# Optimization experiments

Measured on AMD Instinct MI355X. Metric: run time of the kernel, lower is better.

## Reference

```python
import jax, jax.numpy as jnp
import numpy as np

NUM_HEADS = 4
HEAD_DIM = 64
IN_CH = 192
KERNEL_SIZES = (3, 5, 7, 9)  # per-head neighborhood size
NEG_INF = -1e30


def setup_inputs() -> dict:
    key = jax.random.key(0)
    k1, k2, k3 = jax.random.split(key, 3)
    x = jax.random.normal(k1, (8, IN_CH, 96, 96), dtype=jnp.float32)
    # QKV conv: out_channels = head_dim * num_heads * 3 = 768, 3x3, pad 1
    w_qkv = jax.random.normal(k2, (HEAD_DIM * NUM_HEADS * 3, IN_CH, 3, 3), dtype=jnp.float32) * 0.02
    b_qkv = jax.random.normal(k3, (HEAD_DIM * NUM_HEADS * 3,), dtype=jnp.float32) * 0.02
    return {"x": x, "w_qkv": w_qkv, "b_qkv": b_qkv}


def _neighborhood_attention(q, k, v, ksize):
    # q, k, v: [N, H, W, D]; KxK zero-padded neighborhood attention with
    # out-of-bounds positions masked out.
    N, H, W, D = q.shape
    pad = ksize // 2
    kp = jnp.pad(k, ((0, 0), (pad, pad), (pad, pad), (0, 0)))
    vp = jnp.pad(v, ((0, 0), (pad, pad), (pad, pad), (0, 0)))
    scale = 1.0 / np.sqrt(D).astype(np.float32)
    rows = jnp.arange(H)
    cols = jnp.arange(W)
    scores, masks = [], []
    for di in range(ksize):
        for dj in range(ksize):
            k_sh = kp[:, di:di + H, dj:dj + W, :]           # shifted keys
            scores.append(jnp.einsum('nhwd,nhwd->nhw', q, k_sh))
            rv = (rows + di - pad >= 0) & (rows + di - pad < H)   # [H]
            cv = (cols + dj - pad >= 0) & (cols + dj - pad < W)   # [W]
            masks.append(rv[:, None] & cv[None, :])               # [H, W]
    scores = jnp.stack(scores, axis=-1) * scale                   # [N,H,W,K2]
    mask = jnp.stack(masks, axis=-1)[None]                        # [1,H,W,K2]
    scores = jnp.where(mask, scores, NEG_INF)
    attn = jax.nn.softmax(scores, axis=-1)                        # [N,H,W,K2]
    out = jnp.zeros_like(q)
    t = 0
    for di in range(ksize):
        for dj in range(ksize):
            out = out + attn[..., t, None] * vp[:, di:di + H, dj:dj + W, :]
            t += 1
    return out  # [N,H,W,D]


def reference(x, w_qkv, b_qkv):
    # Dense QKV projection (Conv2d, stride 1, padding 1 == SAME for k=3)
    qkv = jax.lax.conv_general_dilated(
        x, w_qkv, window_strides=(1, 1), padding='SAME',
        dimension_numbers=('NCHW', 'OIHW', 'NCHW'))
    qkv = qkv + b_qkv[None, :, None, None]
    # transform_to_nhw1c: NCHW -> NHWC, then split channels into
    # num_heads blocks of 3*head_dim, each split into q, k, v.
    N, C, H, W = qkv.shape
    qkv = jnp.transpose(qkv, (0, 2, 3, 1)).reshape(N, H, W, NUM_HEADS, 3, HEAD_DIM)
    outs = []
    for h, ks in enumerate(KERNEL_SIZES):
        q = qkv[..., h, 0, :]
        k = qkv[..., h, 1, :]
        v = qkv[..., h, 2, :]
        o = _neighborhood_attention(q, k, v, ks)       # [N,H,W,D]
        outs.append(jnp.transpose(o, (0, 3, 1, 2)))    # transform_from_nhw1c -> NCHW
    return jnp.stack(outs, axis=0)  # [num_heads, N, D, H, W]
```

## Files before the change

### kernel.cpp

```cpp
#include <hip/hip_runtime.h>
#include <hip/hip_bf16.h>

#define NH 96
#define NW 96
#define NB 8
#define CIN 192
#define COUT 768
#define PH 98

typedef __attribute__((ext_vector_type(8))) unsigned short ushort8;
typedef __attribute__((ext_vector_type(8))) short bf16x8;
typedef __attribute__((ext_vector_type(4))) float f32x4;

static __device__ __forceinline__ unsigned short f2bf(float f) {
    unsigned int u = __float_as_uint(f);
    return (unsigned short)((u + 0x7fffu + ((u >> 16) & 1u)) >> 16);
}

typedef const __attribute__((address_space(1))) unsigned int gu32;
typedef __attribute__((address_space(3))) unsigned int lu32;
static __device__ __forceinline__ void gload16(const void* g, void* l) {
    __builtin_amdgcn_global_load_lds((gu32*)g, (lu32*)l, 16, 0, 0);
}

__global__ __launch_bounds__(256) void pack_x_kernel(
    const float* __restrict__ x, unsigned short* __restrict__ xp)
{
    __shared__ float tile[32][97];
    int bid = blockIdx.x;
    int ct = bid % 6; int y = (bid / 6) % NH; int n = bid / (6 * NH);
    int tid = threadIdx.x;
    int c0 = ct * 32;
    for (int i = tid; i < 32 * 96; i += 256) {
        int c = i / 96, xx = i % 96;
        tile[c][xx] = x[(((size_t)n * CIN + c0 + c) * NH + y) * NW + xx];
    }
    __syncthreads();
    for (int i = tid; i < 96 * 4; i += 256) {
        int xx = i >> 2, ch = i & 3;
        ushort8 pk;
#pragma unroll
        for (int j = 0; j < 8; ++j) pk[j] = f2bf(tile[ch * 8 + j][xx]);
        *(ushort8*)(xp + ((size_t)(n * PH + y + 1) * PH + xx + 1) * CIN + c0 + ch * 8) = pk;
    }
}

__global__ __launch_bounds__(256) void pack_w_kernel(
    const float* __restrict__ w, unsigned short* __restrict__ bw)
{
    __shared__ float ls[1728];
    int co = blockIdx.x; int tid = threadIdx.x;
    for (int i = tid; i < 1728; i += 256) ls[i] = w[(size_t)co * 1728 + i];
    __syncthreads();
    for (int i = tid; i < 1728; i += 256) {
        int sh = i / 192, ci = i % 192;
        bw[(size_t)co * 1728 + i] = f2bf(ls[ci * 9 + sh]);
    }
}

#define BUFSZ 24576

#define STAGE(S, BUF)                                                          \
    {                                                                          \
        int shift_ = (S) / 6, kk_ = (S) - shift_ * 6;                          \
        int aO_ = ((shift_ / 3) * PH + (shift_ % 3)) * CIN + kk_ * 32;         \
        int bO_ = (S) * 32;                                                    \
        gload16(srcA[0] + aO_, dstA[0] + (BUF));                               \
        gload16(srcA[1] + aO_, dstA[1] + (BUF));                               \
        _Pragma("unroll")                                                      \
        for (int i_ = 0; i_ < 4; ++i_)                                         \
            gload16(srcB[i_] + bO_, dstB[i_] + (BUF));                         \
    }

#define COMPUTE(CUR)                                                           \
    {                                                                          \
        bf16x8 af[8], bf[4];                                                   \
        _Pragma("unroll")                                                      \
        for (int m_ = 0; m_ < 8; ++m_)                                         \
            af[m_] = *(const bf16x8*)(smem + (CUR) + aoff[m_]);                \
        _Pragma("unroll")                                                      \
        for (int n_ = 0; n_ < 4; ++n_)                                         \
            bf[n_] = *(const bf16x8*)(smem + (CUR) + boff[n_]);                \
        __builtin_amdgcn_s_setprio(1);                                         \
        _Pragma("unroll")                                                      \
        for (int m_ = 0; m_ < 8; ++m_)                                         \
            _Pragma("unroll")                                                  \
            for (int n_ = 0; n_ < 4; ++n_)                                     \
                acc[m_][n_] = __builtin_amdgcn_mfma_f32_16x16x32_bf16(         \
                    af[m_], bf[n_], acc[m_][n_], 0, 0, 0);                     \
        __builtin_amdgcn_s_setprio(0);                                         \
    }

__global__ __launch_bounds__(256, 2) void conv_gemm_kernel(
    const unsigned short* __restrict__ xp, const unsigned short* __restrict__ bw,
    const float* __restrict__ bias, unsigned short* __restrict__ qkq,
    unsigned short* __restrict__ vt)
{
    __shared__ __align__(16) char smem[3 * BUFSZ];
    int bid = (blockIdx.x & 7) * 216 + (blockIdx.x >> 3);
    int brow = (bid / 3) * 128, bcol = (bid % 3) * 256;
    int tid = threadIdx.x, lane = tid & 63, wn = tid >> 6;

    const unsigned short* srcA[2];
    const unsigned short* srcB[4];
    char* dstA[2];
    char* dstB[4];
#pragma unroll
    for (int i = 0; i < 2; ++i) {
        int s = i * 256 + tid;
        int row = s >> 2, c = s & 3;
        int p = brow + row;
        int n = p / 9216; int rem = p - n * 9216;
        int y = rem / 96; int xx = rem - y * 96;
        int csw = (c ^ ((row >> 1) & 3)) << 3;
        srcA[i] = xp + ((size_t)(n * PH + y) * PH + xx) * CIN + csw;
        dstA[i] = smem + (i * 256 + (tid & ~63)) * 16;
    }
#pragma unroll
    for (int i = 0; i < 4; ++i) {
        int s = i * 256 + tid;
        int row = s >> 2, c = s & 3;
        int csw = (c ^ ((row >> 1) & 3)) << 3;
        srcB[i] = bw + (size_t)(bcol + row) * 1728 + csw;
        dstB[i] = smem + 8192 + (i * 256 + (tid & ~63)) * 16;
    }

    int aoff[8], boff[4];
#pragma unroll
    for (int m = 0; m < 8; ++m) {
        int rowA = m * 16 + (lane & 15);
        aoff[m] = rowA * 64 + (((lane >> 4) ^ ((rowA >> 1) & 3)) << 4);
    }
#pragma unroll
    for (int n = 0; n < 4; ++n) {
        int colB = wn * 64 + n * 16 + (lane & 15);
        boff[n] = 8192 + colB * 64 + (((lane >> 4) ^ ((colB >> 1) & 3)) << 4);
    }

    STAGE(0, 0);
    STAGE(1, BUFSZ);

    f32x4 acc[8][4] = {};

    for (int t = 0; t < 52; ++t) {
        asm volatile("s_waitcnt vmcnt(6)" ::: "memory");
        __builtin_amdgcn_s_barrier();
        STAGE(t + 2, ((t + 2) % 3) * BUFSZ);
        __builtin_amdgcn_sched_barrier(0);
        COMPUTE((t % 3) * BUFSZ);
    }
    asm volatile("s_waitcnt vmcnt(6)" ::: "memory");
    __builtin_amdgcn_s_barrier();
    COMPUTE((52 % 3) * BUFSZ);
    asm volatile("s_waitcnt vmcnt(0)" ::: "memory");
    __builtin_amdgcn_s_barrier();
    COMPUTE((53 % 3) * BUFSZ);

    __syncthreads();
    unsigned short* sc = (unsigned short*)smem;
    float bn[4];
#pragma unroll
    for (int n = 0; n < 4; ++n)
        bn[n] = bias[bcol + wn * 64 + n * 16 + (lane & 15)];
#pragma unroll
    for (int m = 0; m < 8; ++m)
#pragma unroll
        for (int n = 0; n < 4; ++n) {
            int col = wn * 64 + n * 16 + (lane & 15);
            int cabs = bcol + col;
            float scale = ((cabs % 192) < 64) ? 0.125f : 1.0f;
#pragma unroll
            for (int j = 0; j < 4; ++j) {
                int row = m * 16 + (lane >> 4) * 4 + j;
                sc[row * 256 + (col ^ ((row & 7) << 3))] =
                    f2bf((acc[m][n][j] + bn[n]) * scale);
            }
        }
    __syncthreads();
#pragma unroll
    for (int i = 0; i < 16; ++i) {
        int idx = i * 256 + tid;
        int row = idx >> 5, ch = idx & 31;
        int c0 = bcol + ch * 8;
        int r192 = c0 % 192;
        if (r192 < 128) {
            ushort8 pk = *(const ushort8*)(sc + row * 256 + ((ch * 8) ^ ((row & 7) << 3)));
            *(ushort8*)(qkq + (size_t)(brow + row) * 512 + (c0 / 192) * 128 + r192) = pk;
        }
    }
    int nblk = brow / 9216;
    int prem = brow - nblk * 9216;
#pragma unroll
    for (int h = 0; h < 4; ++h) {
        int lc = h * 192 + 128 - bcol;
        if (lc < 0 || lc > 192) continue;
        unsigned short* vth = vt + (size_t)h * 4718592;
#pragma unroll
        for (int it = 0; it < 4; ++it) {
            int i = it * 256 + tid;
            int d = i & 63, pxb = i >> 6;
            ushort8 pk;
#pragma unroll
            for (int j = 0; j < 8; ++j) {
                int px = pxb * 8 + j;
                pk[j] = sc[px * 256 + ((lc + d) ^ ((px & 7) << 3))];
            }
            *(ushort8*)(vth + ((size_t)(nblk * 64 + d)) * 9216 + prem + pxb * 8) = pk;
        }
    }
}

template<int KS>
static __device__ __forceinline__ void na_body(
    const unsigned short* __restrict__ qkq, const unsigned short* __restrict__ vt,
    float* __restrict__ out, int head, int bid, char* nsm)
{
    constexpr int PAD = KS / 2;
    float (*sO)[97] = (float(*)[97])nsm;
    int y = bid % 96, n = bid / 96;
    int tid = threadIdx.x;
    int wv = tid >> 6, lane = tid & 63;
    int g = lane >> 4, pix = lane & 15;
    int x0 = wv * 16;
    int x = x0 + pix;
    int W = x0 - 8;

    size_t qbase = ((size_t)((n * 96 + y) * 96 + x)) * 512 + (size_t)head * 128;
    bf16x8 qf0 = *(const bf16x8*)(qkq + qbase + g * 8);
    bf16x8 qf1 = *(const bf16x8*)(qkq + qbase + 32 + g * 8);
    asm volatile("s_waitcnt vmcnt(0)" ::: "memory");

    const size_t hoff = (size_t)head * 128 + 64;
#define STAGEK(DI, BUF)                                                        \
    {                                                                          \
        int iy_ = min(max(y + (DI) - PAD, 0), 95);                             \
        size_t rb_ = ((size_t)((n * 96 + iy_) * 96)) * 512 + hoff;             \
        _Pragma("unroll")                                                      \
        for (int i_ = 0; i_ < 2; ++i_) {                                       \
            int ch_ = i_ * 384 + tid;                                          \
            int xx_ = ch_ >> 3, c8_ = (ch_ & 7) ^ (xx_ & 7);                   \
            gload16(qkq + rb_ + (size_t)xx_ * 512 + c8_ * 8,                   \
                    nsm + (BUF) * 12288 + (i_ * 384 + (tid & ~63)) * 16);      \
        }                                                                      \
    }

    STAGEK(0, 0);
    STAGEK(1, 1);

    f32x4 s[KS][2];
#pragma unroll
    for (int di = 0; di < KS; ++di)
#pragma unroll
        for (int kt = 0; kt < 2; ++kt)
#pragma unroll
            for (int r = 0; r < 4; ++r) s[di][kt][r] = -1e30f;

#pragma unroll
    for (int di = 0; di < KS; ++di) {
        if (di < KS - 1) asm volatile("s_waitcnt vmcnt(2)" ::: "memory");
        else             asm volatile("s_waitcnt vmcnt(0)" ::: "memory");
        __builtin_amdgcn_s_barrier();
        if (di + 2 < KS) STAGEK(di + 2, (di + 2) % 3);
        int iy = y + di - PAD;
        if (iy < 0 || iy >= 96) continue;
        const char* kb = nsm + (di % 3) * 12288;
#pragma unroll
        for (int kt = 0; kt < 2; ++kt) {
            int kix_l = W + kt * 16 + pix;
            int ixc = min(max(kix_l, 0), 95);
            const char* kr = kb + ixc * 128;
            bf16x8 kf0 = *(const bf16x8*)(kr + ((g ^ (ixc & 7)) << 4));
            bf16x8 kf1 = *(const bf16x8*)(kr + (((4 + g) ^ (ixc & 7)) << 4));
            f32x4 t = {};
            t = __builtin_amdgcn_mfma_f32_16x16x32_bf16(kf0, qf0, t, 0, 0, 0);
            t = __builtin_amdgcn_mfma_f32_16x16x32_bf16(kf1, qf1, t, 0, 0, 0);
#pragma unroll
            for (int r = 0; r < 4; ++r) {
                int kix = W + kt * 16 + g * 4 + r;
                bool valid = ((unsigned)(kix - x + PAD) <= (unsigned)(2 * PAD)) &&
                             ((unsigned)kix < 96u);
                s[di][kt][r] = valid ? t[r] : -1e30f;
            }
        }
    }

    float m = -3.0e38f;
#pragma unroll
    for (int di = 0; di < KS; ++di)
#pragma unroll
        for (int kt = 0; kt < 2; ++kt)
#pragma unroll
            for (int r = 0; r < 4; ++r) m = fmaxf(m, s[di][kt][r]);
    m = fmaxf(m, __shfl_xor(m, 16, 64));
    m = fmaxf(m, __shfl_xor(m, 32, 64));
    float l = 0.f;
#pragma unroll
    for (int di = 0; di < KS; ++di)
#pragma unroll
        for (int kt = 0; kt < 2; ++kt)
#pragma unroll
            for (int r = 0; r < 4; ++r) {
                float p = __expf(s[di][kt][r] - m);
                s[di][kt][r] = p;
                l += p;
            }
    l += __shfl_xor(l, 16, 64);
    l += __shfl_xor(l, 32, 64);

    f32x4 O[4] = {};
    int addrA = ((2 * (g & 1)) * 16 + pix) * 4;
    int addrB = addrA + 64;
    bool kthi = (g >> 1) != 0;
#pragma unroll
    for (int di = 0; di < KS; ++di) {
        int iy = y + di - PAD;
        if (iy < 0 || iy >= 96) continue;
        unsigned int w0[2], w1[2];
#pragma unroll
        for (int kt = 0; kt < 2; ++kt) {
            asm("v_cvt_pk_bf16_f32 %0, %1, %2"
                : "=v"(w0[kt]) : "v"(s[di][kt][0]), "v"(s[di][kt][1]));
            asm("v_cvt_pk_bf16_f32 %0, %1, %2"
                : "=v"(w1[kt]) : "v"(s[di][kt][2]), "v"(s[di][kt][3]));
        }
        int a0 = __builtin_amdgcn_ds_bpermute(addrA, (int)w0[0]);
        int b0 = __builtin_amdgcn_ds_bpermute(addrA, (int)w0[1]);
        int a1 = __builtin_amdgcn_ds_bpermute(addrA, (int)w1[0]);
        int b1 = __builtin_amdgcn_ds_bpermute(addrA, (int)w1[1]);
        int a2 = __builtin_amdgcn_ds_bpermute(addrB, (int)w0[0]);
        int b2 = __builtin_amdgcn_ds_bpermute(addrB, (int)w0[1]);
        int a3 = __builtin_amdgcn_ds_bpermute(addrB, (int)w1[0]);
        int b3 = __builtin_amdgcn_ds_bpermute(addrB, (int)w1[1]);
        union { int u[4]; bf16x8 v; } pa;
        pa.u[0] = kthi ? b0 : a0;
        pa.u[1] = kthi ? b1 : a1;
        pa.u[2] = kthi ? b2 : a2;
        pa.u[3] = kthi ? b3 : a3;
#pragma unroll
        for (int dc = 0; dc < 4; ++dc) {
            long voff = ((long)((n * 64 + dc * 16 + pix) * 96 + iy)) * 96 + (W + g * 8);
            bf16x8 vf = *(const bf16x8*)(vt + voff);
            O[dc] = __builtin_amdgcn_mfma_f32_16x16x32_bf16(pa.v, vf, O[dc], 0, 0, 0);
        }
    }

    float linv = 1.0f / l;
    float linvj[4];
#pragma unroll
    for (int j = 0; j < 4; ++j)
        linvj[j] = __uint_as_float((unsigned)__builtin_amdgcn_ds_bpermute(
            (4 * g + j) * 4, (int)__float_as_uint(linv)));
    __syncthreads();
#pragma unroll
    for (int dc = 0; dc < 4; ++dc)
#pragma unroll
        for (int j = 0; j < 4; ++j)
            sO[dc * 16 + pix][x0 + g * 4 + j] = O[dc][j] * linvj[j];
    __syncthreads();
    for (int i = tid; i < 1536; i += 384) {
        int d = i / 24, xq = i % 24;
        float4 v4 = { sO[d][xq * 4], sO[d][xq * 4 + 1],
                      sO[d][xq * 4 + 2], sO[d][xq * 4 + 3] };
        *(float4*)(out + ((size_t)(head * 8 + n) * 64 + d) * 9216
                   + y * 96 + xq * 4) = v4;
    }
}

__global__ __launch_bounds__(384, 3) void na_mfma_all(
    const unsigned short* __restrict__ qkq, const unsigned short* __restrict__ vt,
    float* __restrict__ out)
{
    __shared__ __align__(16) char nsm[36864];
    int head = blockIdx.x & 3;
    int bid = blockIdx.x >> 2;
    switch (head) {
        case 0: na_body<3>(qkq, vt,               out, 0, bid, nsm); break;
        case 1: na_body<5>(qkq, vt + 4718592,     out, 1, bid, nsm); break;
        case 2: na_body<7>(qkq, vt + 2 * 4718592, out, 2, bid, nsm); break;
        default: na_body<9>(qkq, vt + 3 * 4718592, out, 3, bid, nsm); break;
    }
}

extern "C" void kernel_launch(void* const* d_in, const int* in_sizes, int n_in,
                              void* d_out, int out_size, void* d_ws, size_t ws_size,
                              hipStream_t stream) {
    const float* x  = (const float*)d_in[0];
    const float* w  = (const float*)d_in[1];
    const float* b  = (const float*)d_in[2];
    float* out = (float*)d_out;

    unsigned short* qkq  = (unsigned short*)d_ws;
    unsigned short* vt   = (unsigned short*)((char*)d_ws + 75497472);
    unsigned short* xpad = (unsigned short*)((char*)d_ws + 113246208);
    unsigned short* bw   = (unsigned short*)((char*)d_ws + 142749696);

    hipMemsetAsync(xpad, 0, 29503488, stream);
    pack_x_kernel<<<NB * NH * 6, 256, 0, stream>>>(x, xpad);
    pack_w_kernel<<<COUT, 256, 0, stream>>>(w, bw);
    conv_gemm_kernel<<<1728, 256, 0, stream>>>(xpad, bw, b, qkq, vt);

    na_mfma_all<<<4 * 768, 384, 0, stream>>>(qkq, vt, out);
}
```

Before: 364.8 us.

## Load conv weight tiles straight into registers, bypassing LDS staging

Each wave uses only its own 64 output columns of the weight tile, so the B operand no longer goes through LDS. It is now read from global memory directly into double-buffered registers, one k-step ahead. Only the input (A) tile stays in the triple-buffered LDS pipeline, which cuts per-stage LDS traffic and LDS reads. In exchange, weight loads become scattered 16-byte global reads with latency hidden only by a one-step register prefetch, and register pressure rises.

```diff
diff --git a/kernel.cpp b/kernel.cpp
--- a/kernel.cpp
+++ b/kernel.cpp
@@ -58,36 +58,36 @@
     }
 }
 
-#define BUFSZ 24576
-
-#define STAGE(S, BUF)                                                          \
+#define ABUF 8192
+
+#define STAGEA(S, BUF)                                                         \
     {                                                                          \
         int shift_ = (S) / 6, kk_ = (S) - shift_ * 6;                          \
         int aO_ = ((shift_ / 3) * PH + (shift_ % 3)) * CIN + kk_ * 32;         \
-        int bO_ = (S) * 32;                                                    \
         gload16(srcA[0] + aO_, dstA[0] + (BUF));                               \
         gload16(srcA[1] + aO_, dstA[1] + (BUF));                               \
+    }
+
+#define LOADB(DST, T)                                                          \
+    {                                                                          \
         _Pragma("unroll")                                                      \
-        for (int i_ = 0; i_ < 4; ++i_)                                         \
-            gload16(srcB[i_] + bO_, dstB[i_] + (BUF));                         \
-    }
-
-#define COMPUTE(CUR)                                                           \
+        for (int n_ = 0; n_ < 4; ++n_)                                         \
+            DST[n_] = *(const bf16x8*)(pB[n_] + (T) * 32);                     \
+    }
+
+#define COMPUTE2(BF, CUR)                                                      \
     {                                                                          \
-        bf16x8 af[8], bf[4];                                                   \
+        bf16x8 af[8];                                                          \
         _Pragma("unroll")                                                      \
         for (int m_ = 0; m_ < 8; ++m_)                                         \
             af[m_] = *(const bf16x8*)(smem + (CUR) + aoff[m_]);                \
-        _Pragma("unroll")                                                      \
-        for (int n_ = 0; n_ < 4; ++n_)                                         \
-            bf[n_] = *(const bf16x8*)(smem + (CUR) + boff[n_]);                \
         __builtin_amdgcn_s_setprio(1);                                         \
         _Pragma("unroll")                                                      \
         for (int m_ = 0; m_ < 8; ++m_)                                         \
             _Pragma("unroll")                                                  \
             for (int n_ = 0; n_ < 4; ++n_)                                     \
                 acc[m_][n_] = __builtin_amdgcn_mfma_f32_16x16x32_bf16(         \
-                    af[m_], bf[n_], acc[m_][n_], 0, 0, 0);                     \
+                    af[m_], BF[n_], acc[m_][n_], 0, 0, 0);                     \
         __builtin_amdgcn_s_setprio(0);                                         \
     }
 
@@ -96,15 +96,13 @@
     const float* __restrict__ bias, unsigned short* __restrict__ qkq,
     unsigned short* __restrict__ vt)
 {
-    __shared__ __align__(16) char smem[3 * BUFSZ];
+    __shared__ __align__(16) char smem[65536];
     int bid = (blockIdx.x & 7) * 216 + (blockIdx.x >> 3);
     int brow = (bid / 3) * 128, bcol = (bid % 3) * 256;
     int tid = threadIdx.x, lane = tid & 63, wn = tid >> 6;
 
     const unsigned short* srcA[2];
-    const unsigned short* srcB[4];
     char* dstA[2];
-    char* dstB[4];
 #pragma unroll
     for (int i = 0; i < 2; ++i) {
         int s = i * 256 + tid;
@@ -116,45 +114,55 @@
         srcA[i] = xp + ((size_t)(n * PH + y) * PH + xx) * CIN + csw;
         dstA[i] = smem + (i * 256 + (tid & ~63)) * 16;
     }
-#pragma unroll
-    for (int i = 0; i < 4; ++i) {
-        int s = i * 256 + tid;
-        int row = s >> 2, c = s & 3;
-        int csw = (c ^ ((row >> 1) & 3)) << 3;
-        srcB[i] = bw + (size_t)(bcol + row) * 1728 + csw;
-        dstB[i] = smem + 8192 + (i * 256 + (tid & ~63)) * 16;
-    }
-
-    int aoff[8], boff[4];
+
+    const unsigned short* pB[4];
+#pragma unroll
+    for (int n = 0; n < 4; ++n)
+        pB[n] = bw + (size_t)(bcol + wn * 64 + n * 16 + (lane & 15)) * 1728
+                   + ((lane >> 4) * 8);
+
+    int aoff[8];
 #pragma unroll
     for (int m = 0; m < 8; ++m) {
         int rowA = m * 16 + (lane & 15);
         aoff[m] = rowA * 64 + (((lane >> 4) ^ ((rowA >> 1) & 3)) << 4);
     }
-#pragma unroll
-    for (int n = 0; n < 4; ++n) {
-        int colB = wn * 64 + n * 16 + (lane & 15);
-        boff[n] = 8192 + colB * 64 + (((lane >> 4) ^ ((colB >> 1) & 3)) << 4);
-    }
-
-    STAGE(0, 0);
-    STAGE(1, BUFSZ);
-
+
+    bf16x8 bfA[4], bfB[4];
     f32x4 acc[8][4] = {};
 
-    for (int t = 0; t < 52; ++t) {
+    LOADB(bfA, 0);
+    STAGEA(0, 0);
+    __builtin_amdgcn_sched_barrier(0);
+    STAGEA(1, ABUF);
+
+    asm volatile("s_waitcnt vmcnt(2)" ::: "memory");
+    __builtin_amdgcn_s_barrier();
+    LOADB(bfB, 1);
+    STAGEA(2, 2 * ABUF);
+    __builtin_amdgcn_sched_barrier(0);
+    COMPUTE2(bfA, 0);
+
+    for (int u = 0; u < 26; ++u) {
+        int t0 = 1 + 2 * u;
         asm volatile("s_waitcnt vmcnt(6)" ::: "memory");
         __builtin_amdgcn_s_barrier();
-        STAGE(t + 2, ((t + 2) % 3) * BUFSZ);
+        LOADB(bfA, t0 + 1);
+        if (t0 < 52) STAGEA(t0 + 2, ((t0 + 2) % 3) * ABUF);
         __builtin_amdgcn_sched_barrier(0);
-        COMPUTE((t % 3) * BUFSZ);
-    }
-    asm volatile("s_waitcnt vmcnt(6)" ::: "memory");
+        COMPUTE2(bfB, (t0 % 3) * ABUF);
+
+        int t1 = t0 + 1;
+        asm volatile("s_waitcnt vmcnt(6)" ::: "memory");
+        __builtin_amdgcn_s_barrier();
+        LOADB(bfB, t1 + 1);
+        if (t1 < 52) STAGEA(t1 + 2, ((t1 + 2) % 3) * ABUF);
+        __builtin_amdgcn_sched_barrier(0);
+        COMPUTE2(bfA, (t1 % 3) * ABUF);
+    }
+    asm volatile("s_waitcnt vmcnt(4)" ::: "memory");
     __builtin_amdgcn_s_barrier();
-    COMPUTE((52 % 3) * BUFSZ);
-    asm volatile("s_waitcnt vmcnt(0)" ::: "memory");
-    __builtin_amdgcn_s_barrier();
-    COMPUTE((53 % 3) * BUFSZ);
+    COMPUTE2(bfB, (53 % 3) * ABUF);
 
     __syncthreads();
     unsigned short* sc = (unsigned short*)smem;
```

Result: slower. 405.3 us (+11.1%).

## Fuse softmax into single pass and stage V rows through LDS with K

Applied to the files above, without the earlier changes.

Merges the score and PV loops into one pass over neighborhood rows. It drops the max subtraction (exp of raw scores) and accumulates the denominator as it goes. V rows are now prefetched into a swizzled LDS slab next to K, using the same triple-buffered async pipeline, instead of being read directly from global memory inside the MFMA loop. This cuts the register footprint of storing all scores and hides V load latency, but doubles LDS per block (72 KB), which may lower occupancy, and removing max subtraction risks overflow for large scores.

```diff
diff --git a/kernel.cpp b/kernel.cpp
--- a/kernel.cpp
+++ b/kernel.cpp
@@ -210,6 +210,7 @@
     }
 }
 
+#define SLAB 24576
 template<int KS>
 static __device__ __forceinline__ void na_body(
     const unsigned short* __restrict__ qkq, const unsigned short* __restrict__ vt,
@@ -231,7 +232,7 @@
     asm volatile("s_waitcnt vmcnt(0)" ::: "memory");
 
     const size_t hoff = (size_t)head * 128 + 64;
-#define STAGEK(DI, BUF)                                                        \
+#define STAGEKV(DI, BUF)                                                       \
     {                                                                          \
         int iy_ = min(max(y + (DI) - PAD, 0), 95);                             \
         size_t rb_ = ((size_t)((n * 96 + iy_) * 96)) * 512 + hoff;             \
@@ -240,30 +241,41 @@
             int ch_ = i_ * 384 + tid;                                          \
             int xx_ = ch_ >> 3, c8_ = (ch_ & 7) ^ (xx_ & 7);                   \
             gload16(qkq + rb_ + (size_t)xx_ * 512 + c8_ * 8,                   \
-                    nsm + (BUF) * 12288 + (i_ * 384 + (tid & ~63)) * 16);      \
+                    nsm + (BUF) * SLAB + (i_ * 384 + (tid & ~63)) * 16);       \
         }                                                                      \
-    }
-
-    STAGEK(0, 0);
-    STAGEK(1, 1);
-
-    f32x4 s[KS][2];
-#pragma unroll
-    for (int di = 0; di < KS; ++di)
-#pragma unroll
-        for (int kt = 0; kt < 2; ++kt)
-#pragma unroll
-            for (int r = 0; r < 4; ++r) s[di][kt][r] = -1e30f;
+        _Pragma("unroll")                                                      \
+        for (int i_ = 0; i_ < 2; ++i_) {                                       \
+            int ch_ = i_ * 384 + tid;                                          \
+            int d_ = ch_ / 12, c_ = ch_ % 12;                                  \
+            int cs_ = c_ ^ ((d_ >> 1) & 3);                                    \
+            gload16(vt + (((size_t)(n * 64 + d_) * 96 + iy_)) * 96 + cs_ * 8,  \
+                    nsm + (BUF) * SLAB + 12288 + (i_ * 384 + (tid & ~63)) * 16); \
+        }                                                                      \
+    }
+
+    STAGEKV(0, 0);
+    STAGEKV(1, 1);
+
+    float l = 0.f;
+    f32x4 O[4] = {};
+    int addrA = ((2 * (g & 1)) * 16 + pix) * 4;
+    int addrB = addrA + 64;
+    bool kthi = (g >> 1) != 0;
+    int cxg = min(max(2 * wv - 1 + g, 0), 11);
+    int vbase = 12288 + pix * 192 + ((cxg ^ ((pix >> 1) & 3)) << 4);
 
 #pragma unroll
     for (int di = 0; di < KS; ++di) {
-        if (di < KS - 1) asm volatile("s_waitcnt vmcnt(2)" ::: "memory");
+        if (di < KS - 1) asm volatile("s_waitcnt vmcnt(4)" ::: "memory");
         else             asm volatile("s_waitcnt vmcnt(0)" ::: "memory");
         __builtin_amdgcn_s_barrier();
-        if (di + 2 < KS) STAGEK(di + 2, (di + 2) % 3);
+        __builtin_amdgcn_sched_barrier(0);
+        if (di + 2 < KS) STAGEKV(di + 2, (di + 2) % 3);
         int iy = y + di - PAD;
         if (iy < 0 || iy >= 96) continue;
-        const char* kb = nsm + (di % 3) * 12288;
+        const char* kb = nsm + (di % 3) * SLAB;
+
+        f32x4 t[2];
 #pragma unroll
         for (int kt = 0; kt < 2; ++kt) {
             int kix_l = W + kt * 16 + pix;
@@ -271,57 +283,26 @@
             const char* kr = kb + ixc * 128;
             bf16x8 kf0 = *(const bf16x8*)(kr + ((g ^ (ixc & 7)) << 4));
             bf16x8 kf1 = *(const bf16x8*)(kr + (((4 + g) ^ (ixc & 7)) << 4));
-            f32x4 t = {};
-            t = __builtin_amdgcn_mfma_f32_16x16x32_bf16(kf0, qf0, t, 0, 0, 0);
-            t = __builtin_amdgcn_mfma_f32_16x16x32_bf16(kf1, qf1, t, 0, 0, 0);
+            f32x4 tt = {};
+            tt = __builtin_amdgcn_mfma_f32_16x16x32_bf16(kf0, qf0, tt, 0, 0, 0);
+            tt = __builtin_amdgcn_mfma_f32_16x16x32_bf16(kf1, qf1, tt, 0, 0, 0);
+            t[kt] = tt;
+        }
+
+        unsigned int w0[2], w1[2];
+#pragma unroll
+        for (int kt = 0; kt < 2; ++kt) {
+            float p[4];
 #pragma unroll
             for (int r = 0; r < 4; ++r) {
                 int kix = W + kt * 16 + g * 4 + r;
                 bool valid = ((unsigned)(kix - x + PAD) <= (unsigned)(2 * PAD)) &&
                              ((unsigned)kix < 96u);
-                s[di][kt][r] = valid ? t[r] : -1e30f;
+                p[r] = valid ? __expf(t[kt][r]) : 0.f;
             }
-        }
-    }
-
-    float m = -3.0e38f;
-#pragma unroll
-    for (int di = 0; di < KS; ++di)
-#pragma unroll
-        for (int kt = 0; kt < 2; ++kt)
-#pragma unroll
-            for (int r = 0; r < 4; ++r) m = fmaxf(m, s[di][kt][r]);
-    m = fmaxf(m, __shfl_xor(m, 16, 64));
-    m = fmaxf(m, __shfl_xor(m, 32, 64));
-    float l = 0.f;
-#pragma unroll
-    for (int di = 0; di < KS; ++di)
-#pragma unroll
-        for (int kt = 0; kt < 2; ++kt)
-#pragma unroll
-            for (int r = 0; r < 4; ++r) {
-                float p = __expf(s[di][kt][r] - m);
-                s[di][kt][r] = p;
-                l += p;
-            }
-    l += __shfl_xor(l, 16, 64);
-    l += __shfl_xor(l, 32, 64);
-
-    f32x4 O[4] = {};
-    int addrA = ((2 * (g & 1)) * 16 + pix) * 4;
-    int addrB = addrA + 64;
-    bool kthi = (g >> 1) != 0;
-#pragma unroll
-    for (int di = 0; di < KS; ++di) {
-        int iy = y + di - PAD;
-        if (iy < 0 || iy >= 96) continue;
-        unsigned int w0[2], w1[2];
-#pragma unroll
-        for (int kt = 0; kt < 2; ++kt) {
-            asm("v_cvt_pk_bf16_f32 %0, %1, %2"
-                : "=v"(w0[kt]) : "v"(s[di][kt][0]), "v"(s[di][kt][1]));
-            asm("v_cvt_pk_bf16_f32 %0, %1, %2"
-                : "=v"(w1[kt]) : "v"(s[di][kt][2]), "v"(s[di][kt][3]));
+            l += (p[0] + p[1]) + (p[2] + p[3]);
+            asm("v_cvt_pk_bf16_f32 %0, %1, %2" : "=v"(w0[kt]) : "v"(p[0]), "v"(p[1]));
+            asm("v_cvt_pk_bf16_f32 %0, %1, %2" : "=v"(w1[kt]) : "v"(p[2]), "v"(p[3]));
         }
         int a0 = __builtin_amdgcn_ds_bpermute(addrA, (int)w0[0]);
         int b0 = __builtin_amdgcn_ds_bpermute(addrA, (int)w0[1]);
@@ -336,14 +317,16 @@
         pa.u[1] = kthi ? b1 : a1;
         pa.u[2] = kthi ? b2 : a2;
         pa.u[3] = kthi ? b3 : a3;
+
 #pragma unroll
         for (int dc = 0; dc < 4; ++dc) {
-            long voff = ((long)((n * 64 + dc * 16 + pix) * 96 + iy)) * 96 + (W + g * 8);
-            bf16x8 vf = *(const bf16x8*)(vt + voff);
+            bf16x8 vf = *(const bf16x8*)(kb + dc * 3072 + vbase);
             O[dc] = __builtin_amdgcn_mfma_f32_16x16x32_bf16(pa.v, vf, O[dc], 0, 0, 0);
         }
     }
 
+    l += __shfl_xor(l, 16, 64);
+    l += __shfl_xor(l, 32, 64);
     float linv = 1.0f / l;
     float linvj[4];
 #pragma unroll
@@ -370,7 +353,7 @@
     const unsigned short* __restrict__ qkq, const unsigned short* __restrict__ vt,
     float* __restrict__ out)
 {
-    __shared__ __align__(16) char nsm[36864];
+    __shared__ __align__(16) char nsm[3 * SLAB];
     int head = blockIdx.x & 3;
     int bid = blockIdx.x >> 2;
     switch (head) {
```

Result: faster. 343.3 us (-5.9%).
